# Performance work log

Hardware: AMD Instinct MI355X
Metric: run time of the kernel (lower is better)

## Reference

```python
import jax, jax.numpy as jnp
import numpy as np

E, T, D, H = 8, 2048, 1024, 4096  # experts, tokens/expert, n_embed, n_mlp_hidden


def setup_inputs() -> dict:
    key = jax.random.key(0)
    ks = jax.random.split(key, 4)
    return {
        "x": jax.random.normal(ks[0], (E, T, D), dtype=jnp.float32),
        "w_c_fc": jax.random.normal(ks[1], (E, D, H), dtype=jnp.float32) * 0.02,
        "b_c_fc": jnp.zeros((E, 1, H), dtype=jnp.float32),
        "w_gate": jax.random.normal(ks[2], (E, D, H), dtype=jnp.float32) * 0.02,
        "b_gate": jnp.zeros((E, 1, H), dtype=jnp.float32),
        "w_c_proj": jax.random.normal(ks[3], (E, H, D), dtype=jnp.float32) * (0.02 * (2 * 12) ** -0.5),
        "b_c_proj": jnp.zeros((E, 1, D), dtype=jnp.float32),
    }


def reference(x, w_c_fc, b_c_fc, w_gate, b_gate, w_c_proj, b_c_proj):
    # Per-expert batched GEMMs with gated activation: silu(h * g)
    h = jnp.einsum('eti,eih->eth', x, w_c_fc) + b_c_fc
    g = jnp.einsum('eti,eih->eth', x, w_gate) + b_gate
    o = jnp.einsum('eth,eho->eto', jax.nn.silu(h * g), w_c_proj) + b_c_proj
    return o
```

## Files before the change

kernel.cpp:

```cpp
#include <hip/hip_runtime.h>
#include <hip/hip_bf16.h>
#include <stdint.h>


#define T_ 2048
#define D_ 1024
#define H_ 4096
#define NE 8

typedef unsigned short u16;
typedef __attribute__((ext_vector_type(8))) u16 u16x8;
typedef __attribute__((ext_vector_type(4))) u16 u16x4;
typedef __attribute__((ext_vector_type(8))) short bf16x8;
typedef __attribute__((ext_vector_type(4))) float f32x4;

__device__ __forceinline__ uint32_t bf16_rne(float f) {
    union { float f; uint32_t u; } v; v.f = f;
    return (v.u + 0x7FFFu + ((v.u >> 16) & 1u)) >> 16;
}

__device__ __forceinline__ void gload16(const void* g, void* l) {
    __builtin_amdgcn_global_load_lds((const __attribute__((address_space(1))) void*)g,
                                     (__attribute__((address_space(3))) void*)l,
                                     16, 0, 0);
}

#define SBAR() __builtin_amdgcn_s_barrier()

__global__ __launch_bounds__(256) void tobf16_kernel(const float* __restrict__ in,
    u16* __restrict__ oh, int n4) {
    int i = blockIdx.x * 256 + threadIdx.x;
    if (i >= n4) return;
    float4 v = reinterpret_cast<const float4*>(in)[i];
    float c[4] = {v.x, v.y, v.z, v.w};
    u16x4 h{};
#pragma unroll
    for (int j = 0; j < 4; ++j) h[j] = (u16)bf16_rne(c[j]);
    reinterpret_cast<u16x4*>(oh)[i] = h;
}

__global__ __launch_bounds__(256) void transpose_hi_kernel(
    const float* __restrict__ in, u16* __restrict__ oh, int R, int C) {
    __shared__ float tile[64][65];
    const int z = blockIdx.z;
    const int r0 = blockIdx.x * 64, c0 = blockIdx.y * 64;
    const float* src = in + (size_t)z * R * C;
    const int tr = threadIdx.x >> 4;
    const int tc = (threadIdx.x & 15) * 4;
#pragma unroll
    for (int j = 0; j < 4; ++j) {
        const float4 v = *reinterpret_cast<const float4*>(&src[(size_t)(r0 + tr + j*16) * C + c0 + tc]);
        tile[tr + j*16][tc+0] = v.x; tile[tr + j*16][tc+1] = v.y;
        tile[tr + j*16][tc+2] = v.z; tile[tr + j*16][tc+3] = v.w;
    }
    __syncthreads();
    const int cl = threadIdx.x & 63;
    const int q  = threadIdx.x >> 6;
    u16x8 h0{}, h1{};
#pragma unroll
    for (int rr = 0; rr < 8; ++rr) h0[rr] = (u16)bf16_rne(tile[q*16 + rr][cl]);
#pragma unroll
    for (int rr = 0; rr < 8; ++rr) h1[rr] = (u16)bf16_rne(tile[q*16 + 8 + rr][cl]);
    size_t ob = ((size_t)z * C + c0 + cl) * R + r0 + q*16;
    *reinterpret_cast<u16x8*>(&oh[ob])     = h0;
    *reinterpret_cast<u16x8*>(&oh[ob + 8]) = h1;
}


template<bool PF, int VM>
__device__ __forceinline__ void fc_step(int tt, u16 (&sm)[4][16384],
    const u16* asrc, const u16* bsrc, const u16* gsrc,
    int adst0, int adst1, int bdst, int gdst,
    int aoff, int boff, int goff,
    f32x4 (&acch)[4][4], f32x4 (&accg)[4][4])
{
    SBAR();
    const u16* sb = &sm[tt & 3][0];
    u16* db = &sm[(tt + 3) & 3][0];
    bf16x8 Af[4], Bf[4], Gf[4];
#pragma unroll
    for (int i = 0; i < 4; ++i) Af[i] = *(const bf16x8*)(sb + aoff + i * 512);
#pragma unroll
    for (int i = 0; i < 4; ++i) Bf[i] = *(const bf16x8*)(sb + boff + i * 512);
    if (PF) {
        gload16(asrc + (tt + 3) * 32, db + adst0);
        gload16(asrc + (tt + 3) * 32 + (size_t)16 * D_, db + adst1);
    }
#pragma unroll
    for (int i = 0; i < 4; ++i) Gf[i] = *(const bf16x8*)(sb + goff + i * 512);
    __builtin_amdgcn_s_setprio(1);
#pragma unroll
    for (int mi = 0; mi < 4; ++mi)
#pragma unroll
        for (int ni = 0; ni < 4; ++ni)
            acch[mi][ni] = __builtin_amdgcn_mfma_f32_16x16x32_bf16(Af[mi], Bf[ni], acch[mi][ni], 0, 0, 0);
    __builtin_amdgcn_s_setprio(0);
    if (PF) {
        gload16(bsrc + (tt + 3) * 32, db + bdst);
        gload16(gsrc + (tt + 3) * 32, db + gdst);
    }
    if (VM == 8)      asm volatile("s_waitcnt vmcnt(8)" ::: "memory");
    else if (VM == 4) asm volatile("s_waitcnt vmcnt(4)" ::: "memory");
    else if (VM == 0) asm volatile("s_waitcnt vmcnt(0)" ::: "memory");
    SBAR();
    __builtin_amdgcn_s_setprio(1);
#pragma unroll
    for (int mi = 0; mi < 4; ++mi)
#pragma unroll
        for (int ni = 0; ni < 4; ++ni)
            accg[mi][ni] = __builtin_amdgcn_mfma_f32_16x16x32_bf16(Af[mi], Gf[ni], accg[mi][ni], 0, 0, 0);
    __builtin_amdgcn_s_setprio(0);
}

__global__ __launch_bounds__(512, 2) void gemm_fc_gate(
    const u16* __restrict__ xh, const u16* __restrict__ fh, const u16* __restrict__ gh,
    const float* __restrict__ bfc, const float* __restrict__ bgt,
    u16* __restrict__ act)
{
    __shared__ __align__(16) u16 sm[4][16384];
    const int z  = blockIdx.z;
    const int lin = blockIdx.x + (blockIdx.y << 3);
    const int swz = ((lin & 7) << 5) + (lin >> 3);
    const int m0 = (swz & 7) * 256;
    const int n0 = (swz >> 3) * 128;
    const int tid = threadIdx.x;
    const int lane = tid & 63;
    const int wid = tid >> 6;
    const int wr = wid >> 1;
    const int wc = wid & 1;

    const int cs = ((lane & 3) ^ ((lane >> 3) & 3)) * 8;
    const u16* asrc = xh + ((size_t)z * T_ + m0 + wid * 32 + (lane >> 2)) * D_ + cs;
    const u16* bsrc = fh + ((size_t)z * H_ + n0 + wid * 16 + (lane >> 2)) * D_ + cs;
    const u16* gsrc = gh + ((size_t)z * H_ + n0 + wid * 16 + (lane >> 2)) * D_ + cs;
    const int adst0 = wid * 1024;
    const int adst1 = adst0 + 512;
    const int bdst  = 8192 + wid * 512;
    const int gdst  = 12288 + wid * 512;

    const int cswz = (((lane & 15) >> 1) & 3);
    const int aoff = (wr * 64 + (lane & 15)) * 32 + ((lane >> 4) ^ cswz) * 8;
    const int boff = 8192 + (wc * 64 + (lane & 15)) * 32 + ((lane >> 4) ^ cswz) * 8;
    const int goff = boff + 4096;

    f32x4 acch[4][4], accg[4][4];
#pragma unroll
    for (int i = 0; i < 4; ++i)
#pragma unroll
        for (int j = 0; j < 4; ++j) {
            acch[i][j] = (f32x4){0.f, 0.f, 0.f, 0.f};
            accg[i][j] = (f32x4){0.f, 0.f, 0.f, 0.f};
        }

#pragma unroll
    for (int u = 0; u < 3; ++u) {
        u16* db = &sm[u][0];
        gload16(asrc + u * 32, db + adst0);
        gload16(asrc + u * 32 + (size_t)16 * D_, db + adst1);
        gload16(bsrc + u * 32, db + bdst);
        gload16(gsrc + u * 32, db + gdst);
    }
    asm volatile("s_waitcnt vmcnt(8)" ::: "memory");

#pragma unroll 4
    for (int t = 0; t < 29; ++t)
        fc_step<true, 8>(t, sm, asrc, bsrc, gsrc, adst0, adst1, bdst, gdst, aoff, boff, goff, acch, accg);
    fc_step<false, 4>(29, sm, asrc, bsrc, gsrc, adst0, adst1, bdst, gdst, aoff, boff, goff, acch, accg);
    fc_step<false, 0>(30, sm, asrc, bsrc, gsrc, adst0, adst1, bdst, gdst, aoff, boff, goff, acch, accg);
    fc_step<false, -1>(31, sm, asrc, bsrc, gsrc, adst0, adst1, bdst, gdst, aoff, boff, goff, acch, accg);

#pragma unroll
    for (int mi = 0; mi < 4; ++mi) {
#pragma unroll
        for (int ni = 0; ni < 4; ++ni) {
            const int col = n0 + wc * 64 + ni * 16 + (lane & 15);
            const float bh = bfc[(size_t)z * H_ + col];
            const float bg = bgt[(size_t)z * H_ + col];
#pragma unroll
            for (int r = 0; r < 4; ++r) {
                const int row = m0 + wr * 64 + mi * 16 + (lane >> 4) * 4 + r;
                float h = acch[mi][ni][r] + bh;
                float g = accg[mi][ni][r] + bg;
                float zz = h * g;
                float s = zz * __builtin_amdgcn_rcpf(1.0f + __expf(-zz));
                act[((size_t)z * T_ + row) * H_ + col] = (u16)bf16_rne(s);
            }
        }
    }
}


template<bool PF, int VM>
__device__ __forceinline__ void pj_step(int tt, u16 (&sm)[4][12288],
    const u16* asrc, const u16* bsrc,
    int adst0, int adst1, int bdst, int aoff, int boff,
    f32x4 (&acc)[4][4])
{
    SBAR();
    const u16* sb = &sm[tt & 3][0];
    u16* db = &sm[(tt + 3) & 3][0];
    bf16x8 Af[4], Bf[4];
#pragma unroll
    for (int i = 0; i < 4; ++i) Af[i] = *(const bf16x8*)(sb + aoff + i * 512);
#pragma unroll
    for (int i = 0; i < 4; ++i) Bf[i] = *(const bf16x8*)(sb + boff + i * 512);
    if (PF) {
        gload16(asrc + (tt + 3) * 32, db + adst0);
        gload16(asrc + (tt + 3) * 32 + (size_t)16 * H_, db + adst1);
        gload16(bsrc + (tt + 3) * 32, db + bdst);
    }
    if (VM == 6)      asm volatile("s_waitcnt vmcnt(6)" ::: "memory");
    else if (VM == 3) asm volatile("s_waitcnt vmcnt(3)" ::: "memory");
    else if (VM == 0) asm volatile("s_waitcnt vmcnt(0)" ::: "memory");
    SBAR();
    __builtin_amdgcn_s_setprio(1);
#pragma unroll
    for (int mi = 0; mi < 4; ++mi)
#pragma unroll
        for (int ni = 0; ni < 4; ++ni)
            acc[mi][ni] = __builtin_amdgcn_mfma_f32_16x16x32_bf16(Af[mi], Bf[ni], acc[mi][ni], 0, 0, 0);
    __builtin_amdgcn_s_setprio(0);
}

__global__ __launch_bounds__(512, 2) void gemm_proj(
    const u16* __restrict__ act, const u16* __restrict__ ph,
    const float* __restrict__ bp, float* __restrict__ out)
{
    __shared__ __align__(16) u16 sm[4][12288];
    const int z  = blockIdx.z;
    const int lin = blockIdx.x + (blockIdx.y << 3);
    const int swz = ((lin & 7) << 3) + (lin >> 3);
    const int m0 = (swz & 7) * 256;
    const int n0 = (swz >> 3) * 128;
    const int tid = threadIdx.x;
    const int lane = tid & 63;
    const int wid = tid >> 6;
    const int wr = wid >> 1;
    const int wc = wid & 1;

    const int cs = ((lane & 3) ^ ((lane >> 3) & 3)) * 8;
    const u16* asrc = act + ((size_t)z * T_ + m0 + wid * 32 + (lane >> 2)) * H_ + cs;
    const u16* bsrc = ph  + ((size_t)z * D_ + n0 + wid * 16 + (lane >> 2)) * H_ + cs;
    const int adst0 = wid * 1024;
    const int adst1 = adst0 + 512;
    const int bdst  = 8192 + wid * 512;

    const int cswz = (((lane & 15) >> 1) & 3);
    const int aoff = (wr * 64 + (lane & 15)) * 32 + ((lane >> 4) ^ cswz) * 8;
    const int boff = 8192 + (wc * 64 + (lane & 15)) * 32 + ((lane >> 4) ^ cswz) * 8;

    f32x4 acc[4][4];
#pragma unroll
    for (int i = 0; i < 4; ++i)
#pragma unroll
        for (int j = 0; j < 4; ++j) acc[i][j] = (f32x4){0.f, 0.f, 0.f, 0.f};

#pragma unroll
    for (int u = 0; u < 3; ++u) {
        u16* db = &sm[u][0];
        gload16(asrc + u * 32, db + adst0);
        gload16(asrc + u * 32 + (size_t)16 * H_, db + adst1);
        gload16(bsrc + u * 32, db + bdst);
    }
    asm volatile("s_waitcnt vmcnt(6)" ::: "memory");

#pragma unroll 4
    for (int t = 0; t < 125; ++t)
        pj_step<true, 6>(t, sm, asrc, bsrc, adst0, adst1, bdst, aoff, boff, acc);
    pj_step<false, 3>(125, sm, asrc, bsrc, adst0, adst1, bdst, aoff, boff, acc);
    pj_step<false, 0>(126, sm, asrc, bsrc, adst0, adst1, bdst, aoff, boff, acc);
    pj_step<false, -1>(127, sm, asrc, bsrc, adst0, adst1, bdst, aoff, boff, acc);

#pragma unroll
    for (int mi = 0; mi < 4; ++mi) {
#pragma unroll
        for (int ni = 0; ni < 4; ++ni) {
            const int col = n0 + wc * 64 + ni * 16 + (lane & 15);
            const float bv = bp[(size_t)z * D_ + col];
#pragma unroll
            for (int r = 0; r < 4; ++r) {
                const int row = m0 + wr * 64 + mi * 16 + (lane >> 4) * 4 + r;
                out[((size_t)z * T_ + row) * D_ + col] = acc[mi][ni][r] + bv;
            }
        }
    }
}

extern "C" void kernel_launch(void* const* d_in, const int* in_sizes, int n_in,
                              void* d_out, int out_size, void* d_ws, size_t ws_size,
                              hipStream_t stream) {
    const float* x   = (const float*)d_in[0];
    const float* wfc = (const float*)d_in[1];
    const float* bfc = (const float*)d_in[2];
    const float* wg  = (const float*)d_in[3];
    const float* bg  = (const float*)d_in[4];
    const float* wp  = (const float*)d_in[5];
    const float* bp  = (const float*)d_in[6];
    float* out = (float*)d_out;

    const size_t per_e = ((size_t)T_*D_ + 3*(size_t)D_*H_ + (size_t)T_*H_) * 2;
    int EB = (int)(ws_size / per_e);
    if (EB < 1) EB = 1;
    if (EB > NE) EB = NE;

    for (int e0 = 0; e0 < NE; e0 += EB) {
        const int eb = (NE - e0 < EB) ? (NE - e0) : EB;
        char* p = (char*)d_ws;
        u16* xh = (u16*)p; p += (size_t)eb*T_*D_*2;
        u16* fh = (u16*)p; p += (size_t)eb*D_*H_*2;
        u16* gh = (u16*)p; p += (size_t)eb*D_*H_*2;
        u16* ph = (u16*)p; p += (size_t)eb*H_*D_*2;
        u16* act = (u16*)p;

        const int n4 = eb * T_ * D_ / 4;
        tobf16_kernel<<<dim3((n4 + 255) / 256), 256, 0, stream>>>(
            x + (size_t)e0*T_*D_, xh, n4);
        transpose_hi_kernel<<<dim3(D_/64, H_/64, eb), 256, 0, stream>>>(
            wfc + (size_t)e0*D_*H_, fh, D_, H_);
        transpose_hi_kernel<<<dim3(D_/64, H_/64, eb), 256, 0, stream>>>(
            wg + (size_t)e0*D_*H_, gh, D_, H_);
        transpose_hi_kernel<<<dim3(H_/64, D_/64, eb), 256, 0, stream>>>(
            wp + (size_t)e0*H_*D_, ph, H_, D_);
        gemm_fc_gate<<<dim3(T_/256, H_/128, eb), 512, 0, stream>>>(
            xh, fh, gh, bfc + (size_t)e0*H_, bg + (size_t)e0*H_, act);
        gemm_proj<<<dim3(T_/256, D_/128, eb), 512, 0, stream>>>(
            act, ph, bp + (size_t)e0*D_, out + (size_t)e0*T_*D_);
    }
}
```

Measured before the change: 616.0 us.

## Software-pipeline LDS fragment reads and widen proj tile to reuse duo-GEMM step

Restructures the fc/gate main loop so the A/B fragments for the next k-step are read from LDS while the current step's MFMAs run, using ping-pong register sets and one barrier per step instead of two. The projection GEMM now uses the same shared step routine by treating its 256-wide N tile as two 128-wide halves, which doubles A reuse per block and halves the proj grid. This aims to hide LDS latency and cut barrier and A-load traffic, at the cost of more registers (extra fragment sets and doubled proj accumulators), which may pressure occupancy at 2 blocks per CU.

```diff
diff --git a/kernel.cpp b/kernel.cpp
--- a/kernel.cpp
+++ b/kernel.cpp
@@ -67,48 +67,51 @@
 }
 
 
-template<bool PF, int VM>
-__device__ __forceinline__ void fc_step(int tt, u16 (&sm)[4][16384],
-    const u16* asrc, const u16* bsrc, const u16* gsrc,
+template<bool PF, bool RD, int VM>
+__device__ __forceinline__ void duo_step(int tt, u16 (*sm)[16384],
+    const u16* asrc, const u16* bsrc, const u16* gsrc, size_t a16str,
     int adst0, int adst1, int bdst, int gdst,
     int aoff, int boff, int goff,
+    bf16x8 (&Ac)[4], bf16x8 (&Bc)[4], bf16x8 (&Gc)[4],
+    bf16x8 (&An)[4], bf16x8 (&Bn)[4],
     f32x4 (&acch)[4][4], f32x4 (&accg)[4][4])
 {
-    SBAR();
-    const u16* sb = &sm[tt & 3][0];
-    u16* db = &sm[(tt + 3) & 3][0];
-    bf16x8 Af[4], Bf[4], Gf[4];
-#pragma unroll
-    for (int i = 0; i < 4; ++i) Af[i] = *(const bf16x8*)(sb + aoff + i * 512);
-#pragma unroll
-    for (int i = 0; i < 4; ++i) Bf[i] = *(const bf16x8*)(sb + boff + i * 512);
-    if (PF) {
-        gload16(asrc + (tt + 3) * 32, db + adst0);
-        gload16(asrc + (tt + 3) * 32 + (size_t)16 * D_, db + adst1);
-    }
-#pragma unroll
-    for (int i = 0; i < 4; ++i) Gf[i] = *(const bf16x8*)(sb + goff + i * 512);
-    __builtin_amdgcn_s_setprio(1);
-#pragma unroll
-    for (int mi = 0; mi < 4; ++mi)
-#pragma unroll
-        for (int ni = 0; ni < 4; ++ni)
-            acch[mi][ni] = __builtin_amdgcn_mfma_f32_16x16x32_bf16(Af[mi], Bf[ni], acch[mi][ni], 0, 0, 0);
-    __builtin_amdgcn_s_setprio(0);
-    if (PF) {
-        gload16(bsrc + (tt + 3) * 32, db + bdst);
-        gload16(gsrc + (tt + 3) * 32, db + gdst);
-    }
-    if (VM == 8)      asm volatile("s_waitcnt vmcnt(8)" ::: "memory");
-    else if (VM == 4) asm volatile("s_waitcnt vmcnt(4)" ::: "memory");
+    if (VM == 4)      asm volatile("s_waitcnt vmcnt(4)" ::: "memory");
     else if (VM == 0) asm volatile("s_waitcnt vmcnt(0)" ::: "memory");
     SBAR();
+    __builtin_amdgcn_sched_barrier(0);
+    const u16* sb = &sm[tt & 3][0];
+    const u16* nb = &sm[(tt + 1) & 3][0];
+    u16* db = &sm[(tt + 3) & 3][0];
+#pragma unroll
+    for (int i = 0; i < 4; ++i) Gc[i] = *(const bf16x8*)(sb + goff + i * 512);
+    if (PF) {
+        gload16(asrc + (size_t)(tt + 3) * 32, db + adst0);
+        gload16(asrc + (size_t)(tt + 3) * 32 + a16str, db + adst1);
+    }
     __builtin_amdgcn_s_setprio(1);
 #pragma unroll
     for (int mi = 0; mi < 4; ++mi)
 #pragma unroll
         for (int ni = 0; ni < 4; ++ni)
-            accg[mi][ni] = __builtin_amdgcn_mfma_f32_16x16x32_bf16(Af[mi], Gf[ni], accg[mi][ni], 0, 0, 0);
+            acch[mi][ni] = __builtin_amdgcn_mfma_f32_16x16x32_bf16(Ac[mi], Bc[ni], acch[mi][ni], 0, 0, 0);
+    __builtin_amdgcn_s_setprio(0);
+    if (RD) {
+#pragma unroll
+        for (int i = 0; i < 4; ++i) An[i] = *(const bf16x8*)(nb + aoff + i * 512);
+#pragma unroll
+        for (int i = 0; i < 4; ++i) Bn[i] = *(const bf16x8*)(nb + boff + i * 512);
+    }
+    if (PF) {
+        gload16(bsrc + (size_t)(tt + 3) * 32, db + bdst);
+        gload16(gsrc + (size_t)(tt + 3) * 32, db + gdst);
+    }
+    __builtin_amdgcn_s_setprio(1);
+#pragma unroll
+    for (int mi = 0; mi < 4; ++mi)
+#pragma unroll
+        for (int ni = 0; ni < 4; ++ni)
+            accg[mi][ni] = __builtin_amdgcn_mfma_f32_16x16x32_bf16(Ac[mi], Gc[ni], accg[mi][ni], 0, 0, 0);
     __builtin_amdgcn_s_setprio(0);
 }
 
@@ -161,13 +164,31 @@
         gload16(gsrc + u * 32, db + gdst);
     }
     asm volatile("s_waitcnt vmcnt(8)" ::: "memory");
-
-#pragma unroll 4
-    for (int t = 0; t < 29; ++t)
-        fc_step<true, 8>(t, sm, asrc, bsrc, gsrc, adst0, adst1, bdst, gdst, aoff, boff, goff, acch, accg);
-    fc_step<false, 4>(29, sm, asrc, bsrc, gsrc, adst0, adst1, bdst, gdst, aoff, boff, goff, acch, accg);
-    fc_step<false, 0>(30, sm, asrc, bsrc, gsrc, adst0, adst1, bdst, gdst, aoff, boff, goff, acch, accg);
-    fc_step<false, -1>(31, sm, asrc, bsrc, gsrc, adst0, adst1, bdst, gdst, aoff, boff, goff, acch, accg);
+    SBAR();
+    __builtin_amdgcn_sched_barrier(0);
+
+    bf16x8 A0[4], B0[4], G0[4], A1[4], B1[4];
+#pragma unroll
+    for (int i = 0; i < 4; ++i) A0[i] = *(const bf16x8*)(&sm[0][0] + aoff + i * 512);
+#pragma unroll
+    for (int i = 0; i < 4; ++i) B0[i] = *(const bf16x8*)(&sm[0][0] + boff + i * 512);
+
+    const size_t a16 = (size_t)16 * D_;
+#pragma unroll 2
+    for (int t = 0; t < 28; t += 2) {
+        duo_step<true, true, 4>(t,   sm, asrc, bsrc, gsrc, a16, adst0, adst1, bdst, gdst,
+                                aoff, boff, goff, A0, B0, G0, A1, B1, acch, accg);
+        duo_step<true, true, 4>(t+1, sm, asrc, bsrc, gsrc, a16, adst0, adst1, bdst, gdst,
+                                aoff, boff, goff, A1, B1, G0, A0, B0, acch, accg);
+    }
+    duo_step<true,  true,  4>(28, sm, asrc, bsrc, gsrc, a16, adst0, adst1, bdst, gdst,
+                              aoff, boff, goff, A0, B0, G0, A1, B1, acch, accg);
+    duo_step<false, true,  4>(29, sm, asrc, bsrc, gsrc, a16, adst0, adst1, bdst, gdst,
+                              aoff, boff, goff, A1, B1, G0, A0, B0, acch, accg);
+    duo_step<false, true,  0>(30, sm, asrc, bsrc, gsrc, a16, adst0, adst1, bdst, gdst,
+                              aoff, boff, goff, A0, B0, G0, A1, B1, acch, accg);
+    duo_step<false, false, -1>(31, sm, asrc, bsrc, gsrc, a16, adst0, adst1, bdst, gdst,
+                              aoff, boff, goff, A1, B1, G0, A0, B0, acch, accg);
 
 #pragma unroll
     for (int mi = 0; mi < 4; ++mi) {
@@ -189,49 +210,15 @@
     }
 }
 
-
-template<bool PF, int VM>
-__device__ __forceinline__ void pj_step(int tt, u16 (&sm)[4][12288],
-    const u16* asrc, const u16* bsrc,
-    int adst0, int adst1, int bdst, int aoff, int boff,
-    f32x4 (&acc)[4][4])
-{
-    SBAR();
-    const u16* sb = &sm[tt & 3][0];
-    u16* db = &sm[(tt + 3) & 3][0];
-    bf16x8 Af[4], Bf[4];
-#pragma unroll
-    for (int i = 0; i < 4; ++i) Af[i] = *(const bf16x8*)(sb + aoff + i * 512);
-#pragma unroll
-    for (int i = 0; i < 4; ++i) Bf[i] = *(const bf16x8*)(sb + boff + i * 512);
-    if (PF) {
-        gload16(asrc + (tt + 3) * 32, db + adst0);
-        gload16(asrc + (tt + 3) * 32 + (size_t)16 * H_, db + adst1);
-        gload16(bsrc + (tt + 3) * 32, db + bdst);
-    }
-    if (VM == 6)      asm volatile("s_waitcnt vmcnt(6)" ::: "memory");
-    else if (VM == 3) asm volatile("s_waitcnt vmcnt(3)" ::: "memory");
-    else if (VM == 0) asm volatile("s_waitcnt vmcnt(0)" ::: "memory");
-    SBAR();
-    __builtin_amdgcn_s_setprio(1);
-#pragma unroll
-    for (int mi = 0; mi < 4; ++mi)
-#pragma unroll
-        for (int ni = 0; ni < 4; ++ni)
-            acc[mi][ni] = __builtin_amdgcn_mfma_f32_16x16x32_bf16(Af[mi], Bf[ni], acc[mi][ni], 0, 0, 0);
-    __builtin_amdgcn_s_setprio(0);
-}
-
 __global__ __launch_bounds__(512, 2) void gemm_proj(
     const u16* __restrict__ act, const u16* __restrict__ ph,
     const float* __restrict__ bp, float* __restrict__ out)
 {
-    __shared__ __align__(16) u16 sm[4][12288];
+    __shared__ __align__(16) u16 sm[4][16384];
     const int z  = blockIdx.z;
-    const int lin = blockIdx.x + (blockIdx.y << 3);
-    const int swz = ((lin & 7) << 3) + (lin >> 3);
-    const int m0 = (swz & 7) * 256;
-    const int n0 = (swz >> 3) * 128;
+    const int lin = blockIdx.x;
+    const int m0 = (lin & 7) * 256;
+    const int n0 = (lin >> 3) * 256;
     const int tid = threadIdx.x;
     const int lane = tid & 63;
     const int wid = tid >> 6;
@@ -241,19 +228,25 @@
     const int cs = ((lane & 3) ^ ((lane >> 3) & 3)) * 8;
     const u16* asrc = act + ((size_t)z * T_ + m0 + wid * 32 + (lane >> 2)) * H_ + cs;
     const u16* bsrc = ph  + ((size_t)z * D_ + n0 + wid * 16 + (lane >> 2)) * H_ + cs;
+    const u16* gsrc = ph  + ((size_t)z * D_ + n0 + 128 + wid * 16 + (lane >> 2)) * H_ + cs;
     const int adst0 = wid * 1024;
     const int adst1 = adst0 + 512;
     const int bdst  = 8192 + wid * 512;
+    const int gdst  = 12288 + wid * 512;
 
     const int cswz = (((lane & 15) >> 1) & 3);
     const int aoff = (wr * 64 + (lane & 15)) * 32 + ((lane >> 4) ^ cswz) * 8;
     const int boff = 8192 + (wc * 64 + (lane & 15)) * 32 + ((lane >> 4) ^ cswz) * 8;
-
-    f32x4 acc[4][4];
+    const int goff = boff + 4096;
+
+    f32x4 acch[4][4], accg[4][4];
 #pragma unroll
     for (int i = 0; i < 4; ++i)
 #pragma unroll
-        for (int j = 0; j < 4; ++j) acc[i][j] = (f32x4){0.f, 0.f, 0.f, 0.f};
+        for (int j = 0; j < 4; ++j) {
+            acch[i][j] = (f32x4){0.f, 0.f, 0.f, 0.f};
+            accg[i][j] = (f32x4){0.f, 0.f, 0.f, 0.f};
+        }
 
 #pragma unroll
     for (int u = 0; u < 3; ++u) {
@@ -261,26 +254,48 @@
         gload16(asrc + u * 32, db + adst0);
         gload16(asrc + u * 32 + (size_t)16 * H_, db + adst1);
         gload16(bsrc + u * 32, db + bdst);
-    }
-    asm volatile("s_waitcnt vmcnt(6)" ::: "memory");
-
-#pragma unroll 4
-    for (int t = 0; t < 125; ++t)
-        pj_step<true, 6>(t, sm, asrc, bsrc, adst0, adst1, bdst, aoff, boff, acc);
-    pj_step<false, 3>(125, sm, asrc, bsrc, adst0, adst1, bdst, aoff, boff, acc);
-    pj_step<false, 0>(126, sm, asrc, bsrc, adst0, adst1, bdst, aoff, boff, acc);
-    pj_step<false, -1>(127, sm, asrc, bsrc, adst0, adst1, bdst, aoff, boff, acc);
+        gload16(gsrc + u * 32, db + gdst);
+    }
+    asm volatile("s_waitcnt vmcnt(8)" ::: "memory");
+    SBAR();
+    __builtin_amdgcn_sched_barrier(0);
+
+    bf16x8 A0[4], B0[4], G0[4], A1[4], B1[4];
+#pragma unroll
+    for (int i = 0; i < 4; ++i) A0[i] = *(const bf16x8*)(&sm[0][0] + aoff + i * 512);
+#pragma unroll
+    for (int i = 0; i < 4; ++i) B0[i] = *(const bf16x8*)(&sm[0][0] + boff + i * 512);
+
+    const size_t a16 = (size_t)16 * H_;
+#pragma unroll 2
+    for (int t = 0; t < 124; t += 2) {
+        duo_step<true, true, 4>(t,   sm, asrc, bsrc, gsrc, a16, adst0, adst1, bdst, gdst,
+                                aoff, boff, goff, A0, B0, G0, A1, B1, acch, accg);
+        duo_step<true, true, 4>(t+1, sm, asrc, bsrc, gsrc, a16, adst0, adst1, bdst, gdst,
+                                aoff, boff, goff, A1, B1, G0, A0, B0, acch, accg);
+    }
+    duo_step<true,  true,  4>(124, sm, asrc, bsrc, gsrc, a16, adst0, adst1, bdst, gdst,
+                              aoff, boff, goff, A0, B0, G0, A1, B1, acch, accg);
+    duo_step<false, true,  4>(125, sm, asrc, bsrc, gsrc, a16, adst0, adst1, bdst, gdst,
+                              aoff, boff, goff, A1, B1, G0, A0, B0, acch, accg);
+    duo_step<false, true,  0>(126, sm, asrc, bsrc, gsrc, a16, adst0, adst1, bdst, gdst,
+                              aoff, boff, goff, A0, B0, G0, A1, B1, acch, accg);
+    duo_step<false, false, -1>(127, sm, asrc, bsrc, gsrc, a16, adst0, adst1, bdst, gdst,
+                              aoff, boff, goff, A1, B1, G0, A0, B0, acch, accg);
 
 #pragma unroll
     for (int mi = 0; mi < 4; ++mi) {
 #pragma unroll
         for (int ni = 0; ni < 4; ++ni) {
-            const int col = n0 + wc * 64 + ni * 16 + (lane & 15);
-            const float bv = bp[(size_t)z * D_ + col];
+            const int colh = n0 + wc * 64 + ni * 16 + (lane & 15);
+            const int colg = colh + 128;
+            const float bvh = bp[(size_t)z * D_ + colh];
+            const float bvg = bp[(size_t)z * D_ + colg];
 #pragma unroll
             for (int r = 0; r < 4; ++r) {
                 const int row = m0 + wr * 64 + mi * 16 + (lane >> 4) * 4 + r;
-                out[((size_t)z * T_ + row) * D_ + col] = acc[mi][ni][r] + bv;
+                out[((size_t)z * T_ + row) * D_ + colh] = acch[mi][ni][r] + bvh;
+                out[((size_t)z * T_ + row) * D_ + colg] = accg[mi][ni][r] + bvg;
             }
         }
     }
@@ -321,9 +336,9 @@
             wg + (size_t)e0*D_*H_, gh, D_, H_);
         transpose_hi_kernel<<<dim3(H_/64, D_/64, eb), 256, 0, stream>>>(
             wp + (size_t)e0*H_*D_, ph, H_, D_);
-        gemm_fc_gate<<<dim3(T_/256, H_/128, eb), 512, 0, stream>>>(
+        gemm_fc_gate<<<dim3(8, 32, eb), 512, 0, stream>>>(
             xh, fh, gh, bfc + (size_t)e0*H_, bg + (size_t)e0*H_, act);
-        gemm_proj<<<dim3(T_/256, D_/128, eb), 512, 0, stream>>>(
+        gemm_proj<<<dim3(32, 1, eb), 512, 0, stream>>>(
             act, ph, bp + (size_t)e0*D_, out + (size_t)e0*T_*D_);
     }
 }
```

New measurement: 582.0 us. 5.5% less time.
